# Kernel optimization log

Measured on AMD Instinct MI355X. Metric: run time of the kernel, lower is better.

Reference implementation:

```python
import jax, jax.numpy as jnp
import numpy as np

B, S, H, E, K = 4, 4096, 2048, 64, 8
SEQ_ALPHA = 0.01


def setup_inputs() -> dict:
    key = jax.random.key(0)
    k1, k2 = jax.random.split(key)
    x = jax.random.normal(k1, (B, S, H), dtype=jnp.float32)
    # kaiming_uniform_(a=sqrt(5)) on [E, H] -> bound = 1/sqrt(H)
    bound = 1.0 / np.sqrt(H)
    weight = jax.random.uniform(k2, (E, H), dtype=jnp.float32, minval=-bound, maxval=bound)
    expert_bias = jnp.zeros((E,), dtype=jnp.float32)
    return {"x": x, "weight": weight, "expert_bias": expert_bias}


def reference(x, weight, expert_bias):
    bsz, seq_len, _ = x.shape
    x_flat = x.reshape(-1, x.shape[-1])                      # [T, H], T = B*S
    logits = x_flat @ weight.T                               # [T, E]
    scores = jax.nn.sigmoid(logits)
    biased_logits = logits + expert_bias[None, :]
    _, topk_idx = jax.lax.top_k(biased_logits, K)            # [T, K] int32
    topk_w = jnp.take_along_axis(scores, topk_idx, axis=-1)  # [T, K]
    topk_w = topk_w / (topk_w.sum(axis=-1, keepdims=True) + 1e-10)  # K > 1
    # load stats (training-mode bincount)
    expert_load = jnp.bincount(topk_idx.reshape(-1), length=E).astype(jnp.int64)
    # sequence-wise balance loss (DeepSeek-V3)
    scores_r = scores.reshape(bsz, seq_len, E)
    expert_mask = jax.nn.one_hot(topk_idx.reshape(bsz, -1), E, dtype=scores.dtype)  # [B, S*K, E]
    f_i = expert_mask.sum(axis=1) / (K * seq_len)            # [B, E]
    normalized = scores_r / (scores_r.sum(axis=2, keepdims=True) + 1e-10)
    P_i = normalized.mean(axis=1)                            # [B, E]
    aux_seq_loss = SEQ_ALPHA * (f_i * P_i).sum(axis=1).mean()
    return (topk_idx, topk_w, aux_seq_loss, expert_load)
```

## Files before the change

kernel.cpp:

```cpp
#include <hip/hip_runtime.h>
#include <math.h>

#define HDIM 2048
#define TTOK 16384
#define NEXP 64
#define TOPK 8
#define SLEN 4096
#define NBATCH 4
#define KSPLIT 4
#define KRANGE 512
#define PARTSZ 1048576

#define OFF_W    131072
#define OFF_LOSS 262144
#define OFF_LOAD 262145

#define WS_PART 262144
#define WS_PACC (WS_PART + 4 * PARTSZ)
#define WS_CACC (WS_PACC + NBATCH * NEXP)

__global__ __launch_bounds__(256) void transpose_w(const float* __restrict__ W,
                                                   float* __restrict__ Wt) {
  __shared__ float tile[64][65];
  const int tid = threadIdx.x;
  const int k0 = blockIdx.x * 64;
  {
    const int kc = (tid & 15) << 2;
    const int er = tid >> 4;
#pragma unroll
    for (int i = 0; i < 4; ++i) {
      int e = er + i * 16;
      float4 v = *(const float4*)(W + (size_t)e * HDIM + k0 + kc);
      tile[e][kc + 0] = v.x; tile[e][kc + 1] = v.y;
      tile[e][kc + 2] = v.z; tile[e][kc + 3] = v.w;
    }
  }
  __syncthreads();
  {
    const int e4 = (tid & 15) << 2;
    const int kr = tid >> 4;
#pragma unroll
    for (int i = 0; i < 4; ++i) {
      int k = kr + i * 16;
      float4 v;
      v.x = tile[e4 + 0][k]; v.y = tile[e4 + 1][k];
      v.z = tile[e4 + 2][k]; v.w = tile[e4 + 3][k];
      *(float4*)(Wt + (size_t)(k0 + k) * NEXP + e4) = v;
    }
  }
}

__global__ __launch_bounds__(512, 8) void gate_gemm(
    const float* __restrict__ x,
    const float* __restrict__ Wt,
    float* __restrict__ part) {
  __shared__ float xs[2][64][64];

  const int tid = threadIdx.x;
  const int lane = tid & 63;
  const int wv = __builtin_amdgcn_readfirstlane(tid >> 6);
  const int kh = blockIdx.x & 3;
  const int tg = blockIdx.x >> 2;
  const int tok0 = tg << 6;
  const int kbase = kh * KRANGE;

  float acc[8] = {0.f, 0.f, 0.f, 0.f, 0.f, 0.f, 0.f, 0.f};

  const int st = tid >> 3;
  const int sg = tid & 7;
  const int swz = st & 15;
  const float* xrow = x + (size_t)(tok0 + st) * HDIM + kbase;

  float4 a0 = *(const float4*)(xrow + (sg << 2));
  float4 a1 = *(const float4*)(xrow + 32 + (sg << 2));

  const int rsw = lane & 15;
  for (int kt = 0; kt < 8; ++kt) {
    float(*xb)[64] = xs[kt & 1];
    *(float4*)&xb[st][(sg ^ swz) << 2] = a0;
    *(float4*)&xb[st][((sg + 8) ^ swz) << 2] = a1;
    __syncthreads();
    if (kt + 1 < 8) {
      const float* nr = xrow + ((kt + 1) << 6);
      a0 = *(const float4*)(nr + (sg << 2));
      a1 = *(const float4*)(nr + 32 + (sg << 2));
    }
    const float* wbase = Wt + (size_t)(kbase + (kt << 6)) * NEXP + (wv << 3);
#pragma unroll
    for (int g = 0; g < 16; ++g) {
      float4 xv4 = *(const float4*)&xb[lane][(g ^ rsw) << 2];
      const float xv[4] = {xv4.x, xv4.y, xv4.z, xv4.w};
#pragma unroll
      for (int i = 0; i < 4; ++i) {
        const float* wr = wbase + (((g << 2) + i) << 6);
#pragma unroll
        for (int j = 0; j < 8; ++j) acc[j] = fmaf(xv[i], wr[j], acc[j]);
      }
    }
  }

  float* dst = part + (size_t)kh * PARTSZ + ((size_t)(wv << 3) << 14) + tok0 + lane;
#pragma unroll
  for (int j = 0; j < 8; ++j) dst[(size_t)j << 14] = acc[j];
}

__global__ __launch_bounds__(256) void gate_epilogue(
    const float* __restrict__ part, const float* __restrict__ bias,
    float* __restrict__ out, float* __restrict__ Pacc,
    float* __restrict__ Cacc) {
  __shared__ float psum[64];
  __shared__ unsigned csum[64];
  const int tid = threadIdx.x;
  const int t = blockIdx.x * 256 + tid;

  if (tid < 64) { psum[tid] = 0.f; csum[tid] = 0u; }
  __syncthreads();

  float bl[64];
  float ssum = 0.f;
#pragma unroll
  for (int e = 0; e < NEXP; ++e) {
    const float* p = part + ((size_t)e << 14) + t;
    float l = p[0] + p[PARTSZ] + p[2 * PARTSZ] + p[3 * PARTSZ];
    ssum += 1.f / (1.f + expf(-l));
    bl[e] = l + bias[e];
  }

  unsigned long long chosen = 0ull;
  int i8[TOPK];
  float w8[TOPK];
  float wsum = 0.f;
#pragma unroll
  for (int j = 0; j < TOPK; ++j) {
    float best = -1e30f;
    int bi = 0;
    float braw = 0.f;
#pragma unroll
    for (int e = 0; e < NEXP; ++e) {
      bool ok = (((chosen >> e) & 1ull) == 0ull) && (bl[e] > best);
      if (ok) { best = bl[e]; bi = e; braw = bl[e] - bias[e]; }
    }
    chosen |= (1ull << bi);
    float sc = 1.f / (1.f + expf(-braw));
    i8[j] = bi;
    w8[j] = sc;
    wsum += sc;
  }
  float inv = 1.f / (wsum + 1e-10f);

  {
    float4 o;
    o.x = (float)i8[0]; o.y = (float)i8[1]; o.z = (float)i8[2]; o.w = (float)i8[3];
    *(float4*)(out + (size_t)t * TOPK) = o;
    o.x = (float)i8[4]; o.y = (float)i8[5]; o.z = (float)i8[6]; o.w = (float)i8[7];
    *(float4*)(out + (size_t)t * TOPK + 4) = o;
    o.x = w8[0] * inv; o.y = w8[1] * inv; o.z = w8[2] * inv; o.w = w8[3] * inv;
    *(float4*)(out + OFF_W + (size_t)t * TOPK) = o;
    o.x = w8[4] * inv; o.y = w8[5] * inv; o.z = w8[6] * inv; o.w = w8[7] * inv;
    *(float4*)(out + OFF_W + (size_t)t * TOPK + 4) = o;
  }

#pragma unroll
  for (int j = 0; j < TOPK; ++j) atomicAdd(&csum[i8[j]], 1u);

  float rinv = 1.f / (ssum + 1e-10f);
#pragma unroll
  for (int e = 0; e < NEXP; ++e) {
    float sc = 1.f / (1.f + expf(-(bl[e] - bias[e])));
    float v = sc * rinv;
#pragma unroll
    for (int off = 32; off; off >>= 1) v += __shfl_xor(v, off);
    if ((tid & 63) == 0) atomicAdd(&psum[e], v);
  }
  __syncthreads();

  if (tid < 64) {
    const int b = blockIdx.x >> 4;
    atomicAdd(&Pacc[(b << 6) + tid], psum[tid]);
    atomicAdd(&Cacc[(b << 6) + tid], (float)csum[tid]);
  }
}

__global__ __launch_bounds__(64) void finalize(const float* __restrict__ Pacc,
                                               const float* __restrict__ Cacc,
                                               float* __restrict__ out) {
  int e = threadIdx.x;
  float load = 0.f, partl = 0.f;
#pragma unroll
  for (int b = 0; b < NBATCH; ++b) {
    float c = Cacc[(b << 6) + e];
    float p = Pacc[(b << 6) + e];
    load += c;
    partl += (c * (1.f / (TOPK * (float)SLEN))) * (p * (1.f / (float)SLEN));
  }
  out[OFF_LOAD + e] = load;
#pragma unroll
  for (int off = 32; off; off >>= 1) partl += __shfl_down(partl, off);
  if (e == 0) out[OFF_LOSS] = 0.01f * partl * (1.f / (float)NBATCH);
}

extern "C" void kernel_launch(void* const* d_in, const int* in_sizes, int n_in,
                              void* d_out, int out_size, void* d_ws, size_t ws_size,
                              hipStream_t stream) {
  const float* x = (const float*)d_in[0];
  const float* W = (const float*)d_in[1];
  const float* bias = (const float*)d_in[2];
  float* out = (float*)d_out;

  float* ws = (float*)d_ws;
  float* Wt = ws;
  float* part = ws + WS_PART;
  float* Pacc = ws + WS_PACC;
  float* Cacc = ws + WS_CACC;

  hipMemsetAsync(Pacc, 0, 2 * NBATCH * NEXP * sizeof(float), stream);
  transpose_w<<<32, 256, 0, stream>>>(W, Wt);
  gate_gemm<<<1024, 512, 0, stream>>>(x, Wt, part);
  gate_epilogue<<<64, 256, 0, stream>>>(part, bias, out, Pacc, Cacc);
  finalize<<<1, 64, 0, stream>>>(Pacc, Cacc, out);
}
```

Before: 280.8 us.

## Retile gate GEMM to 256-token blocks, drop W transpose, fuse finalize into epilogue

The gate GEMM now processes 256 tokens per block, with each thread accumulating 16 experts by 4 tokens. X is transposed into swizzled LDS, and W is read directly from its original layout, so the separate transpose kernel goes away. Two wave halves split the K range and are reduced through LDS. The epilogue stages the summed logits in LDS with coalesced float4 loads, computes P sums per expert column, and uses a last-block atomic counter to do the finalize step, removing one launch. This trades fewer launches and better x reuse for fewer blocks (256), which may reduce occupancy, and for uncoalesced scalar W loads.

```diff
diff --git a/kernel.cpp b/kernel.cpp
--- a/kernel.cpp
+++ b/kernel.cpp
@@ -9,122 +9,158 @@
 #define NBATCH 4
 #define KSPLIT 4
 #define KRANGE 512
-#define PARTSZ 1048576
+#define PARTSZ (NEXP * TTOK)
 
 #define OFF_W    131072
 #define OFF_LOSS 262144
 #define OFF_LOAD 262145
 
-#define WS_PART 262144
-#define WS_PACC (WS_PART + 4 * PARTSZ)
-#define WS_CACC (WS_PACC + NBATCH * NEXP)
-
-__global__ __launch_bounds__(256) void transpose_w(const float* __restrict__ W,
-                                                   float* __restrict__ Wt) {
-  __shared__ float tile[64][65];
-  const int tid = threadIdx.x;
-  const int k0 = blockIdx.x * 64;
-  {
-    const int kc = (tid & 15) << 2;
-    const int er = tid >> 4;
-#pragma unroll
-    for (int i = 0; i < 4; ++i) {
-      int e = er + i * 16;
-      float4 v = *(const float4*)(W + (size_t)e * HDIM + k0 + kc);
-      tile[e][kc + 0] = v.x; tile[e][kc + 1] = v.y;
-      tile[e][kc + 2] = v.z; tile[e][kc + 3] = v.w;
-    }
-  }
-  __syncthreads();
-  {
-    const int e4 = (tid & 15) << 2;
-    const int kr = tid >> 4;
-#pragma unroll
-    for (int i = 0; i < 4; ++i) {
-      int k = kr + i * 16;
-      float4 v;
-      v.x = tile[e4 + 0][k]; v.y = tile[e4 + 1][k];
-      v.z = tile[e4 + 2][k]; v.w = tile[e4 + 3][k];
-      *(float4*)(Wt + (size_t)(k0 + k) * NEXP + e4) = v;
-    }
-  }
-}
-
-__global__ __launch_bounds__(512, 8) void gate_gemm(
+#define WS_PACC 0
+#define WS_CACC 256
+#define WS_CNT  512
+#define WS_PART 1024
+
+__global__ __launch_bounds__(512, 2) void gate_gemm(
     const float* __restrict__ x,
-    const float* __restrict__ Wt,
+    const float* __restrict__ W,
     float* __restrict__ part) {
-  __shared__ float xs[2][64][64];
+  __shared__ float xs[2][32 * 256];
 
   const int tid = threadIdx.x;
   const int lane = tid & 63;
   const int wv = __builtin_amdgcn_readfirstlane(tid >> 6);
-  const int kh = blockIdx.x & 3;
-  const int tg = blockIdx.x >> 2;
-  const int tok0 = tg << 6;
-  const int kbase = kh * KRANGE;
-
-  float acc[8] = {0.f, 0.f, 0.f, 0.f, 0.f, 0.f, 0.f, 0.f};
-
-  const int st = tid >> 3;
-  const int sg = tid & 7;
-  const int swz = st & 15;
-  const float* xrow = x + (size_t)(tok0 + st) * HDIM + kbase;
-
-  float4 a0 = *(const float4*)(xrow + (sg << 2));
-  float4 a1 = *(const float4*)(xrow + 32 + (sg << 2));
-
-  const int rsw = lane & 15;
-  for (int kt = 0; kt < 8; ++kt) {
-    float(*xb)[64] = xs[kt & 1];
-    *(float4*)&xb[st][(sg ^ swz) << 2] = a0;
-    *(float4*)&xb[st][((sg + 8) ^ swz) << 2] = a1;
+  const int eh = wv >> 2;
+  const int eg = wv & 3;
+  const int e0 = eg << 4;
+  const int bid = blockIdx.x;
+  const int kh = bid & 3;
+  const int tg = bid >> 2;
+  const int tok0 = tg << 8;
+  const int kb = kh << 9;
+
+  float4 acc[16];
+#pragma unroll
+  for (int j = 0; j < 16; ++j) acc[j] = make_float4(0.f, 0.f, 0.f, 0.f);
+
+  const int tok_s = tid >> 3;
+  const int kq = tid & 7;
+  const float* xp = x + (size_t)(tok0 + tok_s) * HDIM + kb + (kq << 2);
+
+  float4 a[4];
+#pragma unroll
+  for (int m = 0; m < 4; ++m) a[m] = *(const float4*)(xp + (size_t)(m << 6) * HDIM);
+
+  for (int kt = 0; kt < 16; ++kt) {
+    float* xb = &xs[kt & 1][0];
+    {
+      const int gbase = tok_s >> 2;
+      const int t3 = tok_s & 3;
+#pragma unroll
+      for (int m = 0; m < 4; ++m) {
+        const float* av = (const float*)&a[m];
+        const int g = gbase + (m << 4);
+#pragma unroll
+        for (int i = 0; i < 4; ++i) {
+          const int r = (kq << 2) + i;
+          const int gp = g ^ ((r >> 1) & 7);
+          xb[r * 256 + (gp << 2) + t3] = av[i];
+        }
+      }
+    }
     __syncthreads();
-    if (kt + 1 < 8) {
-      const float* nr = xrow + ((kt + 1) << 6);
-      a0 = *(const float4*)(nr + (sg << 2));
-      a1 = *(const float4*)(nr + 32 + (sg << 2));
-    }
-    const float* wbase = Wt + (size_t)(kbase + (kt << 6)) * NEXP + (wv << 3);
-#pragma unroll
-    for (int g = 0; g < 16; ++g) {
-      float4 xv4 = *(const float4*)&xb[lane][(g ^ rsw) << 2];
-      const float xv[4] = {xv4.x, xv4.y, xv4.z, xv4.w};
-#pragma unroll
-      for (int i = 0; i < 4; ++i) {
-        const float* wr = wbase + (((g << 2) + i) << 6);
-#pragma unroll
-        for (int j = 0; j < 8; ++j) acc[j] = fmaf(xv[i], wr[j], acc[j]);
+    if (kt < 15) {
+      const float* np_ = xp + ((kt + 1) << 5);
+#pragma unroll
+      for (int m = 0; m < 4; ++m)
+        a[m] = *(const float4*)(np_ + (size_t)(m << 6) * HDIM);
+    }
+    const float* wb = W + kb + (kt << 5) + (eh << 4);
+#pragma unroll
+    for (int kk0 = 0; kk0 < 16; kk0 += 4) {
+      float4 xv[4];
+#pragma unroll
+      for (int q = 0; q < 4; ++q) {
+        const int row = (eh << 4) + kk0 + q;
+        xv[q] = *(const float4*)&xb[row * 256 + ((lane ^ ((row >> 1) & 7)) << 2)];
       }
-    }
-  }
-
-  float* dst = part + (size_t)kh * PARTSZ + ((size_t)(wv << 3) << 14) + tok0 + lane;
-#pragma unroll
-  for (int j = 0; j < 8; ++j) dst[(size_t)j << 14] = acc[j];
+#pragma unroll
+      for (int j = 0; j < 16; ++j) {
+        const float* wp = wb + (size_t)(e0 + j) * HDIM + kk0;
+#pragma unroll
+        for (int q = 0; q < 4; ++q) {
+          const float w = wp[q];
+          acc[j].x = fmaf(w, xv[q].x, acc[j].x);
+          acc[j].y = fmaf(w, xv[q].y, acc[j].y);
+          acc[j].z = fmaf(w, xv[q].z, acc[j].z);
+          acc[j].w = fmaf(w, xv[q].w, acc[j].w);
+        }
+      }
+    }
+  }
+
+  __syncthreads();
+  float* rbuf = &xs[0][0];
+  if (eh == 1) {
+    float* dst = rbuf + (eg << 12);
+#pragma unroll
+    for (int j = 0; j < 16; ++j)
+      *(float4*)(dst + j * 256 + (lane << 2)) = acc[j];
+  }
+  __syncthreads();
+  if (eh == 0) {
+    const float* src = rbuf + (eg << 12);
+#pragma unroll
+    for (int j = 0; j < 16; ++j) {
+      float4 o = *(const float4*)(src + j * 256 + (lane << 2));
+      acc[j].x += o.x; acc[j].y += o.y; acc[j].z += o.z; acc[j].w += o.w;
+      *(float4*)(part + (size_t)kh * PARTSZ + (size_t)(e0 + j) * TTOK + tok0 +
+                 (lane << 2)) = acc[j];
+    }
+  }
 }
 
-__global__ __launch_bounds__(256) void gate_epilogue(
+__global__ __launch_bounds__(128) void gate_epilogue(
     const float* __restrict__ part, const float* __restrict__ bias,
     float* __restrict__ out, float* __restrict__ Pacc,
-    float* __restrict__ Cacc) {
-  __shared__ float psum[64];
+    float* __restrict__ Cacc, int* __restrict__ counter) {
+  __shared__ float le[64][132];
+  __shared__ float rinv_sh[128];
   __shared__ unsigned csum[64];
+  __shared__ int lastf;
+
   const int tid = threadIdx.x;
-  const int t = blockIdx.x * 256 + tid;
-
-  if (tid < 64) { psum[tid] = 0.f; csum[tid] = 0u; }
+  const int t0 = blockIdx.x << 7;
+
+  if (tid < 64) csum[tid] = 0u;
+
+#pragma unroll
+  for (int w = 0; w < 16; ++w) {
+    const int idx = (w << 7) + tid;
+    const int e = idx >> 5;
+    const int q = idx & 31;
+    const float* p = part + (size_t)e * TTOK + t0 + (q << 2);
+    float4 s0 = *(const float4*)(p);
+    float4 s1 = *(const float4*)(p + PARTSZ);
+    float4 s2 = *(const float4*)(p + 2 * PARTSZ);
+    float4 s3 = *(const float4*)(p + 3 * PARTSZ);
+    float4 s;
+    s.x = (s0.x + s1.x) + (s2.x + s3.x);
+    s.y = (s0.y + s1.y) + (s2.y + s3.y);
+    s.z = (s0.z + s1.z) + (s2.z + s3.z);
+    s.w = (s0.w + s1.w) + (s2.w + s3.w);
+    *(float4*)&le[e][q << 2] = s;
+  }
   __syncthreads();
 
   float bl[64];
   float ssum = 0.f;
 #pragma unroll
   for (int e = 0; e < NEXP; ++e) {
-    const float* p = part + ((size_t)e << 14) + t;
-    float l = p[0] + p[PARTSZ] + p[2 * PARTSZ] + p[3 * PARTSZ];
+    float l = le[e][tid];
     ssum += 1.f / (1.f + expf(-l));
     bl[e] = l + bias[e];
   }
+  rinv_sh[tid] = 1.f / (ssum + 1e-10f);
 
   unsigned long long chosen = 0ull;
   int i8[TOPK];
@@ -146,8 +182,8 @@
     w8[j] = sc;
     wsum += sc;
   }
-  float inv = 1.f / (wsum + 1e-10f);
-
+  const float inv = 1.f / (wsum + 1e-10f);
+  const int t = t0 + tid;
   {
     float4 o;
     o.x = (float)i8[0]; o.y = (float)i8[1]; o.z = (float)i8[2]; o.w = (float)i8[3];
@@ -159,44 +195,46 @@
     o.x = w8[4] * inv; o.y = w8[5] * inv; o.z = w8[6] * inv; o.w = w8[7] * inv;
     *(float4*)(out + OFF_W + (size_t)t * TOPK + 4) = o;
   }
-
 #pragma unroll
   for (int j = 0; j < TOPK; ++j) atomicAdd(&csum[i8[j]], 1u);
-
-  float rinv = 1.f / (ssum + 1e-10f);
-#pragma unroll
-  for (int e = 0; e < NEXP; ++e) {
-    float sc = 1.f / (1.f + expf(-(bl[e] - bias[e])));
-    float v = sc * rinv;
-#pragma unroll
-    for (int off = 32; off; off >>= 1) v += __shfl_xor(v, off);
-    if ((tid & 63) == 0) atomicAdd(&psum[e], v);
-  }
-  __syncthreads();
-
+  __syncthreads();
+
+  const int b = blockIdx.x >> 5;
   if (tid < 64) {
-    const int b = blockIdx.x >> 4;
-    atomicAdd(&Pacc[(b << 6) + tid], psum[tid]);
+    float p = 0.f;
+    for (int tt = 0; tt < 128; ++tt) {
+      float sc = 1.f / (1.f + expf(-le[tid][tt]));
+      p += sc * rinv_sh[tt];
+    }
+    atomicAdd(&Pacc[(b << 6) + tid], p);
     atomicAdd(&Cacc[(b << 6) + tid], (float)csum[tid]);
   }
-}
-
-__global__ __launch_bounds__(64) void finalize(const float* __restrict__ Pacc,
-                                               const float* __restrict__ Cacc,
-                                               float* __restrict__ out) {
-  int e = threadIdx.x;
-  float load = 0.f, partl = 0.f;
-#pragma unroll
-  for (int b = 0; b < NBATCH; ++b) {
-    float c = Cacc[(b << 6) + e];
-    float p = Pacc[(b << 6) + e];
-    load += c;
-    partl += (c * (1.f / (TOPK * (float)SLEN))) * (p * (1.f / (float)SLEN));
-  }
-  out[OFF_LOAD + e] = load;
-#pragma unroll
-  for (int off = 32; off; off >>= 1) partl += __shfl_down(partl, off);
-  if (e == 0) out[OFF_LOSS] = 0.01f * partl * (1.f / (float)NBATCH);
+  __syncthreads();
+  __threadfence();
+  if (tid == 0) {
+    int old = __hip_atomic_fetch_add(counter, 1, __ATOMIC_ACQ_REL,
+                                     __HIP_MEMORY_SCOPE_AGENT);
+    lastf = (old == 127) ? 1 : 0;
+  }
+  __syncthreads();
+
+  if (lastf && tid < 64) {
+    const int e = tid;
+    float load = 0.f, partl = 0.f;
+#pragma unroll
+    for (int bb = 0; bb < NBATCH; ++bb) {
+      float c = __hip_atomic_load(&Cacc[(bb << 6) + e], __ATOMIC_RELAXED,
+                                  __HIP_MEMORY_SCOPE_AGENT);
+      float p = __hip_atomic_load(&Pacc[(bb << 6) + e], __ATOMIC_RELAXED,
+                                  __HIP_MEMORY_SCOPE_AGENT);
+      load += c;
+      partl += (c * (1.f / (TOPK * (float)SLEN))) * (p * (1.f / (float)SLEN));
+    }
+    out[OFF_LOAD + e] = load;
+#pragma unroll
+    for (int off = 32; off; off >>= 1) partl += __shfl_down(partl, off);
+    if (e == 0) out[OFF_LOSS] = 0.01f * partl * (1.f / (float)NBATCH);
+  }
 }
 
 extern "C" void kernel_launch(void* const* d_in, const int* in_sizes, int n_in,
@@ -208,14 +246,12 @@
   float* out = (float*)d_out;
 
   float* ws = (float*)d_ws;
-  float* Wt = ws;
-  float* part = ws + WS_PART;
   float* Pacc = ws + WS_PACC;
   float* Cacc = ws + WS_CACC;
-
-  hipMemsetAsync(Pacc, 0, 2 * NBATCH * NEXP * sizeof(float), stream);
-  transpose_w<<<32, 256, 0, stream>>>(W, Wt);
-  gate_gemm<<<1024, 512, 0, stream>>>(x, Wt, part);
-  gate_epilogue<<<64, 256, 0, stream>>>(part, bias, out, Pacc, Cacc);
-  finalize<<<1, 64, 0, stream>>>(Pacc, Cacc, out);
+  int* counter = (int*)(ws + WS_CNT);
+  float* part = ws + WS_PART;
+
+  hipMemsetAsync(ws, 0, (WS_CNT + 4) * sizeof(float), stream);
+  gate_gemm<<<256, 512, 0, stream>>>(x, W, part);
+  gate_epilogue<<<128, 128, 0, stream>>>(part, bias, out, Pacc, Cacc, counter);
 }
```

Measured after the change: 388.9 us. 1.38x slower.
